# Performance work log

Measured on AMD Instinct MI355X. Metric: run time of the kernel, lower is better.

Reference implementation:

```python
import jax, jax.numpy as jnp
import numpy as np
from jax import lax

B, S, D = 2, 2048, 1024
DS, K, L = 16, 4, 6
DI = 2 * D          # expand * d_model
V, A = 32000, 7
EPS = 1e-5


def setup_inputs() -> dict:
    key = jax.random.key(0)
    ks = jax.random.split(key, 20)
    g = lambda i, shape, s=0.02: (jax.random.normal(ks[i], shape, dtype=jnp.float32) * s)
    return {
        "features": jax.random.normal(ks[0], (B, S, D), dtype=jnp.float32),
        # per-layer Mamba params, stacked on leading layer dim
        "in_proj_w": g(1, (L, D, 2 * DI)),
        "conv_w": g(2, (L, DI, K), 0.1),
        "conv_b": g(3, (L, DI), 0.0),
        "B_ssm": g(4, (L, DI, DS)),   # fixed analogs of the per-step torch.randn(d_inner,d_state)
        "C_ssm": g(5, (L, DS, DI)),   # fixed analogs of the per-step torch.randn(d_state,d_inner)
        "out_w": g(6, (L, DI, D)),
        "ln_g": jnp.ones((D,), jnp.float32),
        "ln_b": jnp.zeros((D,), jnp.float32),
        # action head (arm: 7-dof, bounds (-1,1))
        "act_w1": g(7, (D, D // 2)), "act_b1": jnp.zeros((D // 2,), jnp.float32),
        "act_w2": g(8, (D // 2, D // 4)), "act_b2": jnp.zeros((D // 4,), jnp.float32),
        "act_w3": g(9, (D // 4, A)), "act_b3": jnp.zeros((A,), jnp.float32),
        # language head
        "lang_w1": g(10, (D, D)), "lang_b1": jnp.zeros((D,), jnp.float32),
        "lang_w2": g(11, (D, V)), "lang_b2": jnp.zeros((V,), jnp.float32),
    }


def _causal_dwconv(x, w, b):
    # x: [B,S,DI], w: [DI,K], b: [DI]  -> causal depthwise conv (torch pad=K-1 then trim)
    lhs = x.transpose(0, 2, 1)                    # [B,DI,S]
    rhs = w[:, None, :]                           # [DI,1,K]
    y = lax.conv_general_dilated(lhs, rhs, window_strides=(1,),
                                 padding=[(K - 1, 0)], feature_group_count=DI,
                                 dimension_numbers=("NCH", "OIH", "NCH"))
    return (y + b[None, :, None]).transpose(0, 2, 1)  # [B,S,DI]


def _selective_scan(xc, Bm, Cm):
    # xc: [B,S,DI]; h_t = 0.9*h_{t-1} + (x_t @ Bm)*0.1 ; y_t = h_t @ Cm
    u = jnp.einsum("bsi,in->bsn", xc, Bm) * 0.1      # [B,S,DS]
    def step(h, u_t):
        h = 0.9 * h + u_t
        return h, h
    _, hs = lax.scan(step, jnp.zeros((xc.shape[0], DS), xc.dtype), u.transpose(1, 0, 2))
    return jnp.einsum("sbn,ni->bsi", hs, Cm)         # [B,S,DI]


def _mamba_block(x, in_w, cw, cb, Bm, Cm, ow):
    xz = jnp.einsum("bsd,do->bso", x, in_w)          # [B,S,2*DI]
    xp, z = xz[..., :DI], xz[..., DI:]
    xc = jax.nn.silu(_causal_dwconv(xp, cw, cb))
    y = _selective_scan(xc, Bm, Cm) * jax.nn.silu(z)
    return jnp.einsum("bsi,id->bsd", y, ow)


def _forward(features, in_proj_w, conv_w, conv_b, B_ssm, C_ssm, out_w,
             ln_g, ln_b, act_w1, act_b1, act_w2, act_b2, act_w3, act_b3,
             lang_w1, lang_b1, lang_w2, lang_b2):
    x = features
    for l in range(L):  # residual Mamba layers (fallback path: x = x + block(x))
        x = x + _mamba_block(x, in_proj_w[l], conv_w[l], conv_b[l],
                             B_ssm[l], C_ssm[l], out_w[l])
    mu = jnp.mean(x, -1, keepdims=True)
    var = jnp.mean(jnp.square(x - mu), -1, keepdims=True)
    x = (x - mu) * lax.rsqrt(var + EPS) * ln_g + ln_b
    # action head: bounds (-1,1) => affine rescale is identity
    h = jax.nn.relu(x @ act_w1 + act_b1)
    h = jax.nn.relu(h @ act_w2 + act_b2)
    actions = jnp.tanh(h @ act_w3 + act_b3)
    # language head
    logits = jax.nn.relu(x @ lang_w1 + lang_b1) @ lang_w2 + lang_b2
    return actions, logits


def reference(features, in_proj_w, conv_w, conv_b, B_ssm, C_ssm, out_w,
              ln_g, ln_b, act_w1, act_b1, act_w2, act_b2, act_w3, act_b3,
              lang_w1, lang_b1, lang_w2, lang_b2):
    return _forward(features, in_proj_w, conv_w, conv_b, B_ssm, C_ssm, out_w,
                    ln_g, ln_b, act_w1, act_b1, act_w2, act_b2, act_w3, act_b3,
                    lang_w1, lang_b1, lang_w2, lang_b2)
```

## Files before the change

### kernel.cpp

```cpp
#include <hip/hip_runtime.h>
#include <hip/hip_bf16.h>
#include <cstdint>
#include <cstddef>

#define TT 4096
#define SS 2048
#define DD 1024
#define DDI 2048
#define LL 6
#define VV 32000
#define AA 7

typedef __hip_bfloat16 bf16;
typedef __attribute__((ext_vector_type(8))) short bf16x8;
typedef __attribute__((ext_vector_type(4))) float f32x4;

typedef const __attribute__((address_space(1))) void* gas_ptr;
typedef __attribute__((address_space(3))) void* las_ptr;

static __device__ __forceinline__ float b2f(bf16 h) { return __bfloat162float(h); }
static __device__ __forceinline__ bf16 f2b(float f) { return __float2bfloat16(f); }

#define SWZ(off) ((off) ^ ((((off) >> 7) & 3) << 4))

template<int EPI>
__global__ __launch_bounds__(512, 2)
void g8_k(const bf16* __restrict__ A, const bf16* __restrict__ Wt,
          int K, int mx, int out_ld,
          float* __restrict__ of32, bf16* __restrict__ ob16,
          const float* __restrict__ bias)
{
    extern __shared__ char lds[];
    const int nwg = gridDim.x;
    int l = blockIdx.x;
    if ((nwg & 7) == 0) l = (l & 7) * (nwg >> 3) + (l >> 3);
    const int row0 = (l % mx) * 256, col0 = (l / mx) * 256;

    const int tid = threadIdx.x, wid = tid >> 6, lane = tid & 63;
    const int wr = wid >> 2, wc = wid & 3;
    const int l15 = lane & 15, kq = lane >> 4;

    f32x4 acc[8][4];
#pragma unroll
    for (int m = 0; m < 8; ++m)
#pragma unroll
        for (int n = 0; n < 4; ++n) acc[m][n] = f32x4{0.f, 0.f, 0.f, 0.f};

    const int sr   = tid >> 2;
    const int colE = (((tid & 3) ^ ((tid >> 3) & 3)) * 8);
    const bf16* gA = A  + (size_t)(row0 + sr) * K + colE;
    const bf16* gB = Wt + (size_t)(col0 + sr) * K + colE;
    const int dst0 = tid * 16, dst1 = 8192 + tid * 16;

    auto stageA = [&](int kh) {
        char* b = lds + (kh & 3) * 16384;
        __builtin_amdgcn_global_load_lds((gas_ptr)(gA + kh * 32),                   (las_ptr)(b + dst0), 16, 0, 0);
        __builtin_amdgcn_global_load_lds((gas_ptr)(gA + (size_t)128 * K + kh * 32), (las_ptr)(b + dst1), 16, 0, 0);
    };
    auto stageB = [&](int kh) {
        char* b = lds + 65536 + (kh & 3) * 16384;
        __builtin_amdgcn_global_load_lds((gas_ptr)(gB + kh * 32),                   (las_ptr)(b + dst0), 16, 0, 0);
        __builtin_amdgcn_global_load_lds((gas_ptr)(gB + (size_t)128 * K + kh * 32), (las_ptr)(b + dst1), 16, 0, 0);
    };

    const int NT = K >> 6, KH = K >> 5;
    stageA(0); stageB(0); stageA(1); stageB(1);
    stageA(2); stageB(2); stageA(3); stageB(3);
    int nextA = 4, nextB = 4;

    for (int t = 0; t < NT; ++t) {
        const char* As0 = lds + ((2 * t) & 3) * 16384;
        const char* As1 = lds + ((2 * t + 1) & 3) * 16384;
        const char* Bs0 = lds + 65536 + ((2 * t) & 3) * 16384;
        const char* Bs1 = lds + 65536 + ((2 * t + 1) & 3) * 16384;
        bf16x8 af[4], bfg[4];

        if (t < NT - 3) asm volatile("s_waitcnt vmcnt(10)" ::: "memory");
        else            asm volatile("s_waitcnt vmcnt(0)" ::: "memory");
        __builtin_amdgcn_sched_barrier(0);
        __builtin_amdgcn_s_barrier();
        __builtin_amdgcn_sched_barrier(0);
#pragma unroll
        for (int fn = 0; fn < 4; ++fn)
            bfg[fn] = *(const bf16x8*)(Bs0 + SWZ((wc * 64 + fn * 16 + l15) * 64 + kq * 16));
#pragma unroll
        for (int fm = 0; fm < 4; ++fm)
            af[fm] = *(const bf16x8*)(As0 + SWZ((wr * 128 + fm * 16 + l15) * 64 + kq * 16));
        if (t > 0 && nextA < KH) { stageA(nextA); ++nextA; }
        asm volatile("s_waitcnt lgkmcnt(0)" ::: "memory");
        __builtin_amdgcn_sched_barrier(0);
        __builtin_amdgcn_s_setprio(1);
#pragma unroll
        for (int fm = 0; fm < 4; ++fm)
#pragma unroll
            for (int fn = 0; fn < 4; ++fn)
                acc[fm][fn] = __builtin_amdgcn_mfma_f32_16x16x32_bf16(af[fm], bfg[fn], acc[fm][fn], 0, 0, 0);
        __builtin_amdgcn_s_setprio(0);
        __builtin_amdgcn_sched_barrier(0);
        __builtin_amdgcn_s_barrier();
        __builtin_amdgcn_sched_barrier(0);

#pragma unroll
        for (int fm = 0; fm < 4; ++fm)
            af[fm] = *(const bf16x8*)(As0 + SWZ((wr * 128 + 64 + fm * 16 + l15) * 64 + kq * 16));
        if (nextB < KH) { stageB(nextB); ++nextB; }
        asm volatile("s_waitcnt lgkmcnt(0)" ::: "memory");
        __builtin_amdgcn_sched_barrier(0);
        __builtin_amdgcn_s_setprio(1);
#pragma unroll
        for (int fm = 0; fm < 4; ++fm)
#pragma unroll
            for (int fn = 0; fn < 4; ++fn)
                acc[4 + fm][fn] = __builtin_amdgcn_mfma_f32_16x16x32_bf16(af[fm], bfg[fn], acc[4 + fm][fn], 0, 0, 0);
        __builtin_amdgcn_s_setprio(0);
        __builtin_amdgcn_sched_barrier(0);
        __builtin_amdgcn_s_barrier();
        __builtin_amdgcn_sched_barrier(0);

        if (t < NT - 3) asm volatile("s_waitcnt vmcnt(10)" ::: "memory");
        else            asm volatile("s_waitcnt vmcnt(0)" ::: "memory");
        __builtin_amdgcn_sched_barrier(0);
        __builtin_amdgcn_s_barrier();
        __builtin_amdgcn_sched_barrier(0);
#pragma unroll
        for (int fn = 0; fn < 4; ++fn)
            bfg[fn] = *(const bf16x8*)(Bs1 + SWZ((wc * 64 + fn * 16 + l15) * 64 + kq * 16));
#pragma unroll
        for (int fm = 0; fm < 4; ++fm)
            af[fm] = *(const bf16x8*)(As1 + SWZ((wr * 128 + fm * 16 + l15) * 64 + kq * 16));
        if (nextA < KH) { stageA(nextA); ++nextA; }
        asm volatile("s_waitcnt lgkmcnt(0)" ::: "memory");
        __builtin_amdgcn_sched_barrier(0);
        __builtin_amdgcn_s_setprio(1);
#pragma unroll
        for (int fm = 0; fm < 4; ++fm)
#pragma unroll
            for (int fn = 0; fn < 4; ++fn)
                acc[fm][fn] = __builtin_amdgcn_mfma_f32_16x16x32_bf16(af[fm], bfg[fn], acc[fm][fn], 0, 0, 0);
        __builtin_amdgcn_s_setprio(0);
        __builtin_amdgcn_sched_barrier(0);
        __builtin_amdgcn_s_barrier();
        __builtin_amdgcn_sched_barrier(0);

#pragma unroll
        for (int fm = 0; fm < 4; ++fm)
            af[fm] = *(const bf16x8*)(As1 + SWZ((wr * 128 + 64 + fm * 16 + l15) * 64 + kq * 16));
        if (nextB < KH) { stageB(nextB); ++nextB; }
        asm volatile("s_waitcnt lgkmcnt(0)" ::: "memory");
        __builtin_amdgcn_sched_barrier(0);
        __builtin_amdgcn_s_setprio(1);
#pragma unroll
        for (int fm = 0; fm < 4; ++fm)
#pragma unroll
            for (int fn = 0; fn < 4; ++fn)
                acc[4 + fm][fn] = __builtin_amdgcn_mfma_f32_16x16x32_bf16(af[fm], bfg[fn], acc[4 + fm][fn], 0, 0, 0);
        __builtin_amdgcn_s_setprio(0);
        __builtin_amdgcn_sched_barrier(0);
        __builtin_amdgcn_s_barrier();
        __builtin_amdgcn_sched_barrier(0);
    }

#pragma unroll
    for (int fm = 0; fm < 8; ++fm) {
#pragma unroll
        for (int fn = 0; fn < 4; ++fn) {
#pragma unroll
            for (int r = 0; r < 4; ++r) {
                const int row = row0 + wr * 128 + fm * 16 + kq * 4 + r;
                const int col = col0 + wc * 64 + fn * 16 + l15;
                float v = acc[fm][fn][r];
                if (EPI == 0) ob16[(size_t)row * out_ld + col] = f2b(v);
                else          of32[(size_t)row * out_ld + col] = v + bias[col];
            }
        }
    }
}

template<int EPI>
__global__ __launch_bounds__(256)
void gemm_k(const bf16* __restrict__ A, const bf16* __restrict__ Wt,
            int K, int out_ld,
            float* __restrict__ of32, bf16* __restrict__ ob16,
            const float* __restrict__ bias,
            const bf16* __restrict__ zp, int z_ld)
{
    __shared__ bf16x8 lsA8[128 * 4];
    __shared__ bf16x8 lsB8[128 * 4];
    bf16* lsA = (bf16*)lsA8;
    bf16* lsB = (bf16*)lsB8;

    const int tid  = threadIdx.x;
    const int w    = tid >> 6;
    const int lane = tid & 63;
    const int row0 = blockIdx.x * 128;
    const int col0 = blockIdx.y * 128;
    const int wr   = (w >> 1) * 64;
    const int wc   = (w & 1) * 64;
    const int l15  = lane & 15;
    const int kq   = lane >> 4;

    f32x4 acc[4][4];
#pragma unroll
    for (int m = 0; m < 4; ++m)
#pragma unroll
        for (int n = 0; n < 4; ++n) acc[m][n] = f32x4{0.f, 0.f, 0.f, 0.f};

    const int s0 = tid, s1 = tid + 256;
    const size_t ga0 = (size_t)(row0 + (s0 >> 2)) * K + (s0 & 3) * 8;
    const size_t ga1 = (size_t)(row0 + (s1 >> 2)) * K + (s1 & 3) * 8;
    const size_t gb0 = (size_t)(col0 + (s0 >> 2)) * K + (s0 & 3) * 8;
    const size_t gb1 = (size_t)(col0 + (s1 >> 2)) * K + (s1 & 3) * 8;
    bf16* la0 = lsA + (size_t)(w * 64) * 8;
    bf16* la1 = lsA + (size_t)(256 + w * 64) * 8;
    bf16* lb0 = lsB + (size_t)(w * 64) * 8;
    bf16* lb1 = lsB + (size_t)(256 + w * 64) * 8;

    for (int k0 = 0; k0 < K; k0 += 32) {
        __builtin_amdgcn_global_load_lds((gas_ptr)(A  + ga0 + k0), (las_ptr)la0, 16, 0, 0);
        __builtin_amdgcn_global_load_lds((gas_ptr)(A  + ga1 + k0), (las_ptr)la1, 16, 0, 0);
        __builtin_amdgcn_global_load_lds((gas_ptr)(Wt + gb0 + k0), (las_ptr)lb0, 16, 0, 0);
        __builtin_amdgcn_global_load_lds((gas_ptr)(Wt + gb1 + k0), (las_ptr)lb1, 16, 0, 0);
        __syncthreads();

        bf16x8 af[4], bfr[4];
#pragma unroll
        for (int m = 0; m < 4; ++m)
            af[m] = *(const bf16x8*)(lsA + (size_t)(wr + m * 16 + l15) * 32 + kq * 8);
#pragma unroll
        for (int n = 0; n < 4; ++n)
            bfr[n] = *(const bf16x8*)(lsB + (size_t)(wc + n * 16 + l15) * 32 + kq * 8);
#pragma unroll
        for (int m = 0; m < 4; ++m)
#pragma unroll
            for (int n = 0; n < 4; ++n)
                acc[m][n] = __builtin_amdgcn_mfma_f32_16x16x32_bf16(af[m], bfr[n], acc[m][n], 0, 0, 0);
        __syncthreads();
    }

#pragma unroll
    for (int m = 0; m < 4; ++m) {
#pragma unroll
        for (int n = 0; n < 4; ++n) {
#pragma unroll
            for (int r = 0; r < 4; ++r) {
                const int row = row0 + wr + m * 16 + kq * 4 + r;
                const int col = col0 + wc + n * 16 + l15;
                float v = acc[m][n][r];
                if (EPI == 2) {
                    float zf = b2f(zp[(size_t)row * z_ld + col]);
                    v *= zf / (1.f + expf(-zf));
                    ob16[(size_t)row * out_ld + col] = f2b(v);
                } else if (EPI == 3) {
                    float rr = of32[(size_t)row * out_ld + col] + v;
                    of32[(size_t)row * out_ld + col] = rr;
                    ob16[(size_t)row * out_ld + col] = f2b(rr);
                } else if (EPI == 4) {
                    v = fmaxf(v + bias[col], 0.f);
                    ob16[(size_t)row * out_ld + col] = f2b(v);
                }
            }
        }
    }
}

__global__ __launch_bounds__(256)
void usk_k(const bf16* __restrict__ A, const bf16* __restrict__ Wt,
           float* __restrict__ up)
{
    __shared__ bf16x8 lsA8[128 * 4];
    __shared__ bf16x8 lsB8[128 * 4];
    bf16* lsA = (bf16*)lsA8;
    bf16* lsB = (bf16*)lsB8;
    const int K = 2048;

    const int tid  = threadIdx.x;
    const int w    = tid >> 6;
    const int lane = tid & 63;
    const int row0 = blockIdx.x * 128;
    const int spl  = blockIdx.y;
    const int kbeg = spl * 256;
    const int wr   = (w >> 1) * 64;
    const int wc   = (w & 1) * 64;
    const int l15  = lane & 15;
    const int kq   = lane >> 4;

    f32x4 acc[4][4];
#pragma unroll
    for (int m = 0; m < 4; ++m)
#pragma unroll
        for (int n = 0; n < 4; ++n) acc[m][n] = f32x4{0.f, 0.f, 0.f, 0.f};

    const int s0 = tid, s1 = tid + 256;
    const size_t ga0 = (size_t)(row0 + (s0 >> 2)) * K + (s0 & 3) * 8;
    const size_t ga1 = (size_t)(row0 + (s1 >> 2)) * K + (s1 & 3) * 8;
    const size_t gb0 = (size_t)(s0 >> 2) * K + (s0 & 3) * 8;
    const size_t gb1 = (size_t)(s1 >> 2) * K + (s1 & 3) * 8;
    bf16* la0 = lsA + (size_t)(w * 64) * 8;
    bf16* la1 = lsA + (size_t)(256 + w * 64) * 8;
    bf16* lb0 = lsB + (size_t)(w * 64) * 8;
    bf16* lb1 = lsB + (size_t)(256 + w * 64) * 8;

    for (int k0 = kbeg; k0 < kbeg + 256; k0 += 32) {
        __builtin_amdgcn_global_load_lds((gas_ptr)(A  + ga0 + k0), (las_ptr)la0, 16, 0, 0);
        __builtin_amdgcn_global_load_lds((gas_ptr)(A  + ga1 + k0), (las_ptr)la1, 16, 0, 0);
        __builtin_amdgcn_global_load_lds((gas_ptr)(Wt + gb0 + k0), (las_ptr)lb0, 16, 0, 0);
        __builtin_amdgcn_global_load_lds((gas_ptr)(Wt + gb1 + k0), (las_ptr)lb1, 16, 0, 0);
        __syncthreads();

        bf16x8 af[4], bfr[4];
#pragma unroll
        for (int m = 0; m < 4; ++m)
            af[m] = *(const bf16x8*)(lsA + (size_t)(wr + m * 16 + l15) * 32 + kq * 8);
#pragma unroll
        for (int n = 0; n < 4; ++n)
            bfr[n] = *(const bf16x8*)(lsB + (size_t)(wc + n * 16 + l15) * 32 + kq * 8);
#pragma unroll
        for (int m = 0; m < 4; ++m)
#pragma unroll
            for (int n = 0; n < 4; ++n)
                acc[m][n] = __builtin_amdgcn_mfma_f32_16x16x32_bf16(af[m], bfr[n], acc[m][n], 0, 0, 0);
        __syncthreads();
    }

    if (wc == 0) {
#pragma unroll
        for (int m = 0; m < 4; ++m)
#pragma unroll
            for (int r = 0; r < 4; ++r) {
                const int row = row0 + wr + m * 16 + kq * 4 + r;
                up[(size_t)spl * TT * 16 + (size_t)row * 16 + l15] = acc[m][0][r];
            }
    }
}

__global__ void ured_k(const float* __restrict__ up, float* __restrict__ u)
{
    int i = blockIdx.x * 256 + threadIdx.x;
    float s = 0.f;
#pragma unroll
    for (int k = 0; k < 8; ++k) s += up[(size_t)k * TT * 16 + i];
    u[i] = s;
}

__global__ __launch_bounds__(256)
void transpose_k(const float* __restrict__ W, bf16* __restrict__ WT, int K, int N)
{
    __shared__ bf16 t[64][66];
    const int k0 = blockIdx.x * 64, n0 = blockIdx.y * 64;
    const int tid = threadIdx.x;
#pragma unroll
    for (int i = 0; i < 16; ++i) {
        int idx = i * 256 + tid;
        int kk = idx >> 6, nn = idx & 63;
        t[nn][kk] = f2b(W[(size_t)(k0 + kk) * N + n0 + nn]);
    }
    __syncthreads();
#pragma unroll
    for (int i = 0; i < 16; ++i) {
        int idx = i * 256 + tid;
        int nn = idx >> 6, kk = idx & 63;
        WT[(size_t)(n0 + nn) * K + k0 + kk] = t[nn][kk];
    }
}

__global__ void prep_bm_k(const float* __restrict__ Bm, bf16* __restrict__ BmT)
{
    int idx = blockIdx.x * 256 + threadIdx.x;
    int n = idx >> 11, k = idx & 2047;
    float v = (n < 16) ? Bm[(size_t)k * 16 + n] * 0.1f : 0.f;
    BmT[idx] = f2b(v);
}

__global__ void prep_cm_k(const float* __restrict__ Cm, bf16* __restrict__ CmT)
{
    int idx = blockIdx.x * 256 + threadIdx.x;
    int i = idx >> 5, k = idx & 31;
    float v = (k < 16) ? Cm[(size_t)k * 2048 + i] : 0.f;
    CmT[idx] = f2b(v);
}

__global__ void copyfeat_k(const float* __restrict__ f, float* __restrict__ xf,
                           bf16* __restrict__ xb)
{
    int i = (blockIdx.x * 256 + threadIdx.x) * 4;
    float4 v = *(const float4*)(f + i);
    *(float4*)(xf + i) = v;
    xb[i + 0] = f2b(v.x);
    xb[i + 1] = f2b(v.y);
    xb[i + 2] = f2b(v.z);
    xb[i + 3] = f2b(v.w);
}

__global__ void conv_k(const bf16* __restrict__ xz, const float* __restrict__ cw,
                       const float* __restrict__ cb, bf16* __restrict__ xc)
{
    int idx = blockIdx.x * 256 + threadIdx.x;
    int t = idx >> 11, i = idx & 2047;
    int s = t & (SS - 1);
    float4 wv = *(const float4*)(cw + i * 4);
    float acc = cb[i];
    const bf16* base = xz + (size_t)t * 4096 + i;
    if (s >= 3) {
        acc = fmaf(b2f(base[-3 * 4096]), wv.x, acc);
        acc = fmaf(b2f(base[-2 * 4096]), wv.y, acc);
        acc = fmaf(b2f(base[-1 * 4096]), wv.z, acc);
    } else {
        if (s >= 2) acc = fmaf(b2f(base[-2 * 4096]), wv.y, acc);
        if (s >= 1) acc = fmaf(b2f(base[-1 * 4096]), wv.z, acc);
    }
    acc = fmaf(b2f(base[0]), wv.w, acc);
    float sig = 1.f / (1.f + expf(-acc));
    xc[idx] = f2b(acc * sig);
}

__global__ void scan2_k(const float* __restrict__ u, bf16* __restrict__ hs)
{
    int gid = blockIdx.x * 256 + threadIdx.x;
    int n = gid & 15, c = (gid >> 4) & 63, b = gid >> 10;
    int start = c * 32;
    const float* ub = u + (size_t)b * SS * 16;
    bf16* hb = hs + (size_t)b * SS * 32;
    float h = 0.f;
    int w0 = start - 96; if (w0 < 0) w0 = 0;
    for (int t = w0; t < start; ++t) h = 0.9f * h + ub[(size_t)t * 16 + n];
    const bf16 zero = f2b(0.f);
    for (int t = start; t < start + 32; ++t) {
        h = 0.9f * h + ub[(size_t)t * 16 + n];
        hb[(size_t)t * 32 + n] = f2b(h);
        hb[(size_t)t * 32 + 16 + n] = zero;
    }
}

__global__ __launch_bounds__(256)
void ln_k(const float* __restrict__ x, const float* __restrict__ g,
          const float* __restrict__ bb, bf16* __restrict__ xn)
{
    int t = blockIdx.x, tid = threadIdx.x;
    const float* xr = x + (size_t)t * DD;
    float4 v = *(const float4*)(xr + tid * 4);
    float s = v.x + v.y + v.z + v.w;
#pragma unroll
    for (int o = 32; o > 0; o >>= 1) s += __shfl_down(s, o, 64);
    __shared__ float r1[4], r2[4];
    if ((tid & 63) == 0) r1[tid >> 6] = s;
    __syncthreads();
    float mu = (r1[0] + r1[1] + r1[2] + r1[3]) * (1.f / DD);
    float d0 = v.x - mu, d1 = v.y - mu, d2 = v.z - mu, d3 = v.w - mu;
    float ss = d0 * d0 + d1 * d1 + d2 * d2 + d3 * d3;
#pragma unroll
    for (int o = 32; o > 0; o >>= 1) ss += __shfl_down(ss, o, 64);
    if ((tid & 63) == 0) r2[tid >> 6] = ss;
    __syncthreads();
    float var = (r2[0] + r2[1] + r2[2] + r2[3]) * (1.f / DD);
    float inv = rsqrtf(var + 1e-5f);
    int di = tid * 4;
    xn[(size_t)t * DD + di + 0] = f2b(d0 * inv * g[di + 0] + bb[di + 0]);
    xn[(size_t)t * DD + di + 1] = f2b(d1 * inv * g[di + 1] + bb[di + 1]);
    xn[(size_t)t * DD + di + 2] = f2b(d2 * inv * g[di + 2] + bb[di + 2]);
    xn[(size_t)t * DD + di + 3] = f2b(d3 * inv * g[di + 3] + bb[di + 3]);
}

__global__ void act3_k(const bf16* __restrict__ h2, const float* __restrict__ w3,
                       const float* __restrict__ b3, float* __restrict__ out)
{
    int idx = blockIdx.x * 256 + threadIdx.x;
    if (idx >= TT * AA) return;
    int t = idx / AA, a = idx - t * AA;
    float acc = b3[a];
    const bf16* hr = h2 + (size_t)t * 256;
    for (int k = 0; k < 256; ++k)
        acc = fmaf(b2f(hr[k]), w3[k * AA + a], acc);
    out[idx] = tanhf(acc);
}

extern "C" void kernel_launch(void* const* d_in, const int* in_sizes, int n_in,
                              void* d_out, int out_size, void* d_ws, size_t ws_size,
                              hipStream_t stream)
{
    (void)in_sizes; (void)n_in; (void)out_size; (void)ws_size;
    const float* features = (const float*)d_in[0];
    const float* in_proj_w = (const float*)d_in[1];
    const float* conv_w = (const float*)d_in[2];
    const float* conv_b = (const float*)d_in[3];
    const float* B_ssm = (const float*)d_in[4];
    const float* C_ssm = (const float*)d_in[5];
    const float* out_w = (const float*)d_in[6];
    const float* ln_g = (const float*)d_in[7];
    const float* ln_b = (const float*)d_in[8];
    const float* act_w1 = (const float*)d_in[9];
    const float* act_b1 = (const float*)d_in[10];
    const float* act_w2 = (const float*)d_in[11];
    const float* act_b2 = (const float*)d_in[12];
    const float* act_w3 = (const float*)d_in[13];
    const float* act_b3 = (const float*)d_in[14];
    const float* lang_w1 = (const float*)d_in[15];
    const float* lang_b1 = (const float*)d_in[16];
    const float* lang_w2 = (const float*)d_in[17];
    const float* lang_b2 = (const float*)d_in[18];

    static bool attr_done = false;
    if (!attr_done) {
        hipFuncSetAttribute((const void*)&g8_k<0>, hipFuncAttributeMaxDynamicSharedMemorySize, 131072);
        hipFuncSetAttribute((const void*)&g8_k<5>, hipFuncAttributeMaxDynamicSharedMemorySize, 131072);
        attr_done = true;
    }

    char* p = (char*)d_ws;
    size_t off = 0;
    auto alloc = [&](size_t bytes) -> void* {
        void* q = p + off;
        off = (off + bytes + 255) & ~(size_t)255;
        return q;
    };
    float* x_f  = (float*)alloc((size_t)TT * DD * 4);
    bf16*  x_b  = (bf16*) alloc((size_t)TT * DD * 2);
    bf16*  xz   = (bf16*) alloc((size_t)TT * 4096 * 2);
    bf16*  xc   = (bf16*) alloc((size_t)TT * DDI * 2);
    float* u    = (float*)alloc((size_t)TT * 16 * 4);
    float* up   = (float*)alloc((size_t)8 * TT * 16 * 4);
    bf16*  hs   = (bf16*) alloc((size_t)TT * 32 * 2);
    bf16*  xn   = (bf16*) alloc((size_t)TT * DD * 2);
    bf16*  h1   = (bf16*) alloc((size_t)TT * 512 * 2);
    bf16*  h2   = (bf16*) alloc((size_t)TT * 256 * 2);
    bf16*  hl   = (bf16*) alloc((size_t)TT * DD * 2);
    bf16*  inwT = (bf16*) alloc((size_t)LL * 4096 * 1024 * 2);
    bf16*  owT  = (bf16*) alloc((size_t)LL * 1024 * 2048 * 2);
    bf16*  bmT  = (bf16*) alloc((size_t)LL * 128 * 2048 * 2);
    bf16*  cmT  = (bf16*) alloc((size_t)LL * 2048 * 32 * 2);
    bf16*  a1T  = (bf16*) alloc((size_t)512 * 1024 * 2);
    bf16*  a2T  = (bf16*) alloc((size_t)256 * 512 * 2);
    bf16*  l1T  = (bf16*) alloc((size_t)1024 * 1024 * 2);
    bf16*  l2T  = (bf16*) alloc((size_t)VV * 1024 * 2);
    bf16*  y    = xc;

    copyfeat_k<<<TT * DD / 1024, 256, 0, stream>>>(features, x_f, x_b);
    for (int l = 0; l < LL; ++l) {
        transpose_k<<<dim3(16, 64), 256, 0, stream>>>(in_proj_w + (size_t)l * 1024 * 4096,
                                                      inwT + (size_t)l * 4096 * 1024, 1024, 4096);
        transpose_k<<<dim3(32, 16), 256, 0, stream>>>(out_w + (size_t)l * 2048 * 1024,
                                                      owT + (size_t)l * 1024 * 2048, 2048, 1024);
        prep_bm_k<<<(128 * 2048) / 256, 256, 0, stream>>>(B_ssm + (size_t)l * 2048 * 16,
                                                          bmT + (size_t)l * 128 * 2048);
        prep_cm_k<<<(2048 * 32) / 256, 256, 0, stream>>>(C_ssm + (size_t)l * 16 * 2048,
                                                         cmT + (size_t)l * 2048 * 32);
    }
    transpose_k<<<dim3(16, 8), 256, 0, stream>>>(act_w1, a1T, 1024, 512);
    transpose_k<<<dim3(8, 4), 256, 0, stream>>>(act_w2, a2T, 512, 256);
    transpose_k<<<dim3(16, 16), 256, 0, stream>>>(lang_w1, l1T, 1024, 1024);
    transpose_k<<<dim3(16, 500), 256, 0, stream>>>(lang_w2, l2T, 1024, VV);

    for (int l = 0; l < LL; ++l) {
        g8_k<0><<<256, 512, 131072, stream>>>(x_b, inwT + (size_t)l * 4096 * 1024,
                                              1024, 16, 4096, nullptr, xz, nullptr);
        conv_k<<<TT * DDI / 256, 256, 0, stream>>>(xz, conv_w + (size_t)l * DDI * 4,
                                                   conv_b + (size_t)l * DDI, xc);
        usk_k<<<dim3(32, 8), 256, 0, stream>>>(xc, bmT + (size_t)l * 128 * 2048, up);
        ured_k<<<TT * 16 / 256, 256, 0, stream>>>(up, u);
        scan2_k<<<8, 256, 0, stream>>>(u, hs);
        gemm_k<2><<<dim3(32, 16), 256, 0, stream>>>(hs, cmT + (size_t)l * 2048 * 32,
                                                    32, 2048, nullptr, y, nullptr, xz + 2048, 4096);
        gemm_k<3><<<dim3(32, 8), 256, 0, stream>>>(y, owT + (size_t)l * 1024 * 2048,
                                                   2048, 1024, x_f, x_b, nullptr, nullptr, 0);
    }

    ln_k<<<TT, 256, 0, stream>>>(x_f, ln_g, ln_b, xn);
    gemm_k<4><<<dim3(32, 4), 256, 0, stream>>>(xn, a1T, 1024, 512, nullptr, h1, act_b1, nullptr, 0);
    gemm_k<4><<<dim3(32, 2), 256, 0, stream>>>(h1, a2T, 512, 256, nullptr, h2, act_b2, nullptr, 0);
    act3_k<<<(TT * AA + 255) / 256, 256, 0, stream>>>(h2, act_w3, act_b3, (float*)d_out);
    gemm_k<4><<<dim3(32, 8), 256, 0, stream>>>(xn, l1T, 1024, 1024, nullptr, hl, lang_b1, nullptr, 0);
    g8_k<5><<<2000, 512, 131072, stream>>>(hl, l2T, 1024, 16, VV,
                                           (float*)d_out + (size_t)TT * AA, nullptr, lang_b2);
}
```

Measured before the change: 1.646 ms.

## Pipeline out-projection GEMM with async LDS loads; compute C-projection with fp32 FMA kernel

Replaces the padded K=32 MFMA GEMM for the SSM output projection (hs @ Cm with SiLU(z) gating) with a simple per-token fp32 FMA kernel that reads C_ssm directly. This removes the per-layer Cm transpose/padding prep and the hs zero padding. The out-projection residual GEMM moves from the synchronous 128x128 gemm_k to a new g8h_k kernel. g8h_k uses global_load_lds into a 5-stage swizzled LDS ring with vmcnt-based waits and setprio around the MFMAs, to overlap loads with compute. The cost is higher LDS use per block (80 KB) and more complex wait logic.

```diff
diff --git a/kernel.cpp b/kernel.cpp
--- a/kernel.cpp
+++ b/kernel.cpp
@@ -20,6 +20,10 @@
 
 static __device__ __forceinline__ float b2f(bf16 h) { return __bfloat162float(h); }
 static __device__ __forceinline__ bf16 f2b(float f) { return __float2bfloat16(f); }
+static __device__ __forceinline__ float bs2f(short x) {
+    unsigned int u = ((unsigned int)(unsigned short)x) << 16;
+    float f; __builtin_memcpy(&f, &u, 4); return f;
+}
 
 #define SWZ(off) ((off) ^ ((((off) >> 7) & 3) << 4))
 
@@ -177,12 +181,105 @@
 }
 
 template<int EPI>
+__global__ __launch_bounds__(256, 2)
+void g8h_k(const bf16* __restrict__ A, const bf16* __restrict__ Wt,
+           int K, int mx, int out_ld,
+           float* __restrict__ of32, bf16* __restrict__ ob16,
+           const float* __restrict__ bias)
+{
+    extern __shared__ char lds[];
+    const int nwg = gridDim.x;
+    int l = blockIdx.x;
+    if ((nwg & 7) == 0) l = (l & 7) * (nwg >> 3) + (l >> 3);
+    const int row0 = (l % mx) * 128, col0 = (l / mx) * 128;
+
+    const int tid = threadIdx.x, wid = tid >> 6, lane = tid & 63;
+    const int wr = wid >> 1, wc = wid & 1;
+    const int l15 = lane & 15, kq = lane >> 4;
+
+    f32x4 acc[4][4];
+#pragma unroll
+    for (int m = 0; m < 4; ++m)
+#pragma unroll
+        for (int n = 0; n < 4; ++n) acc[m][n] = f32x4{0.f, 0.f, 0.f, 0.f};
+
+    const int sr   = tid >> 2;
+    const int colE = (((tid & 3) ^ ((tid >> 3) & 3)) * 8);
+    const bf16* gA = A  + (size_t)(row0 + sr) * K + colE;
+    const bf16* gB = Wt + (size_t)(col0 + sr) * K + colE;
+    const int dst0 = tid * 16, dst1 = 4096 + tid * 16;
+
+    auto stage = [&](int kh) {
+        char* a = lds + (kh % 5) * 8192;
+        char* b = lds + 40960 + (kh % 5) * 8192;
+        __builtin_amdgcn_global_load_lds((gas_ptr)(gA + kh * 32),                  (las_ptr)(a + dst0), 16, 0, 0);
+        __builtin_amdgcn_global_load_lds((gas_ptr)(gA + (size_t)64 * K + kh * 32), (las_ptr)(a + dst1), 16, 0, 0);
+        __builtin_amdgcn_global_load_lds((gas_ptr)(gB + kh * 32),                  (las_ptr)(b + dst0), 16, 0, 0);
+        __builtin_amdgcn_global_load_lds((gas_ptr)(gB + (size_t)64 * K + kh * 32), (las_ptr)(b + dst1), 16, 0, 0);
+    };
+
+    const int KH = K >> 5;
+    stage(0); stage(1); stage(2); stage(3);
+
+    for (int kh = 0; kh < KH; ++kh) {
+        const int rem = KH - 1 - kh;
+        if (rem >= 3)      asm volatile("s_waitcnt vmcnt(12)" ::: "memory");
+        else if (rem == 2) asm volatile("s_waitcnt vmcnt(8)" ::: "memory");
+        else if (rem == 1) asm volatile("s_waitcnt vmcnt(4)" ::: "memory");
+        else               asm volatile("s_waitcnt vmcnt(0)" ::: "memory");
+        __builtin_amdgcn_sched_barrier(0);
+        __builtin_amdgcn_s_barrier();
+        __builtin_amdgcn_sched_barrier(0);
+
+        const char* As = lds + (kh % 5) * 8192;
+        const char* Bs = lds + 40960 + (kh % 5) * 8192;
+        bf16x8 af[4], bfg[4];
+#pragma unroll
+        for (int fn = 0; fn < 4; ++fn)
+            bfg[fn] = *(const bf16x8*)(Bs + SWZ((wc * 64 + fn * 16 + l15) * 64 + kq * 16));
+#pragma unroll
+        for (int fm = 0; fm < 4; ++fm)
+            af[fm] = *(const bf16x8*)(As + SWZ((wr * 64 + fm * 16 + l15) * 64 + kq * 16));
+        if (kh + 4 < KH) stage(kh + 4);
+        asm volatile("s_waitcnt lgkmcnt(0)" ::: "memory");
+        __builtin_amdgcn_sched_barrier(0);
+        __builtin_amdgcn_s_setprio(1);
+#pragma unroll
+        for (int fm = 0; fm < 4; ++fm)
+#pragma unroll
+            for (int fn = 0; fn < 4; ++fn)
+                acc[fm][fn] = __builtin_amdgcn_mfma_f32_16x16x32_bf16(af[fm], bfg[fn], acc[fm][fn], 0, 0, 0);
+        __builtin_amdgcn_s_setprio(0);
+        __builtin_amdgcn_sched_barrier(0);
+    }
+
+#pragma unroll
+    for (int fm = 0; fm < 4; ++fm) {
+#pragma unroll
+        for (int fn = 0; fn < 4; ++fn) {
+#pragma unroll
+            for (int r = 0; r < 4; ++r) {
+                const int row = row0 + wr * 64 + fm * 16 + kq * 4 + r;
+                const int col = col0 + wc * 64 + fn * 16 + l15;
+                float v = acc[fm][fn][r];
+                if (EPI == 3) {
+                    float rr = of32[(size_t)row * out_ld + col] + v;
+                    of32[(size_t)row * out_ld + col] = rr;
+                    ob16[(size_t)row * out_ld + col] = f2b(rr);
+                } else {
+                    ob16[(size_t)row * out_ld + col] = f2b(v);
+                }
+            }
+        }
+    }
+}
+
+template<int EPI>
 __global__ __launch_bounds__(256)
 void gemm_k(const bf16* __restrict__ A, const bf16* __restrict__ Wt,
             int K, int out_ld,
             float* __restrict__ of32, bf16* __restrict__ ob16,
-            const float* __restrict__ bias,
-            const bf16* __restrict__ zp, int z_ld)
+            const float* __restrict__ bias)
 {
     __shared__ bf16x8 lsA8[128 * 4];
     __shared__ bf16x8 lsB8[128 * 4];
@@ -246,18 +343,8 @@
                 const int row = row0 + wr + m * 16 + kq * 4 + r;
                 const int col = col0 + wc + n * 16 + l15;
                 float v = acc[m][n][r];
-                if (EPI == 2) {
-                    float zf = b2f(zp[(size_t)row * z_ld + col]);
-                    v *= zf / (1.f + expf(-zf));
-                    ob16[(size_t)row * out_ld + col] = f2b(v);
-                } else if (EPI == 3) {
-                    float rr = of32[(size_t)row * out_ld + col] + v;
-                    of32[(size_t)row * out_ld + col] = rr;
-                    ob16[(size_t)row * out_ld + col] = f2b(rr);
-                } else if (EPI == 4) {
-                    v = fmaxf(v + bias[col], 0.f);
-                    ob16[(size_t)row * out_ld + col] = f2b(v);
-                }
+                v = fmaxf(v + bias[col], 0.f);
+                ob16[(size_t)row * out_ld + col] = f2b(v);
             }
         }
     }
@@ -369,14 +456,6 @@
     int n = idx >> 11, k = idx & 2047;
     float v = (n < 16) ? Bm[(size_t)k * 16 + n] * 0.1f : 0.f;
     BmT[idx] = f2b(v);
-}
-
-__global__ void prep_cm_k(const float* __restrict__ Cm, bf16* __restrict__ CmT)
-{
-    int idx = blockIdx.x * 256 + threadIdx.x;
-    int i = idx >> 5, k = idx & 31;
-    float v = (k < 16) ? Cm[(size_t)k * 2048 + i] : 0.f;
-    CmT[idx] = f2b(v);
 }
 
 __global__ void copyfeat_k(const float* __restrict__ f, float* __restrict__ xf,
@@ -413,21 +492,45 @@
     xc[idx] = f2b(acc * sig);
 }
 
-__global__ void scan2_k(const float* __restrict__ u, bf16* __restrict__ hs)
+__global__ void scan2_k(const float* __restrict__ u, float* __restrict__ hs)
 {
     int gid = blockIdx.x * 256 + threadIdx.x;
     int n = gid & 15, c = (gid >> 4) & 63, b = gid >> 10;
     int start = c * 32;
     const float* ub = u + (size_t)b * SS * 16;
-    bf16* hb = hs + (size_t)b * SS * 32;
+    float* hb = hs + (size_t)b * SS * 16;
     float h = 0.f;
     int w0 = start - 96; if (w0 < 0) w0 = 0;
     for (int t = w0; t < start; ++t) h = 0.9f * h + ub[(size_t)t * 16 + n];
-    const bf16 zero = f2b(0.f);
     for (int t = start; t < start + 32; ++t) {
         h = 0.9f * h + ub[(size_t)t * 16 + n];
-        hb[(size_t)t * 32 + n] = f2b(h);
-        hb[(size_t)t * 32 + 16 + n] = zero;
+        hb[(size_t)t * 16 + n] = h;
+    }
+}
+
+__global__ __launch_bounds__(256)
+void yk_k(const float* __restrict__ hs, const float* __restrict__ Cm,
+          const bf16* __restrict__ xz, bf16* __restrict__ y)
+{
+    const int t = blockIdx.x, i0 = threadIdx.x * 8;
+    const float* h = hs + (size_t)t * 16;
+    float o[8] = {0.f, 0.f, 0.f, 0.f, 0.f, 0.f, 0.f, 0.f};
+#pragma unroll
+    for (int n = 0; n < 16; ++n) {
+        float hn = h[n];
+        const float4* c = (const float4*)(Cm + (size_t)n * DDI + i0);
+        float4 c0 = c[0], c1 = c[1];
+        o[0] = fmaf(hn, c0.x, o[0]); o[1] = fmaf(hn, c0.y, o[1]);
+        o[2] = fmaf(hn, c0.z, o[2]); o[3] = fmaf(hn, c0.w, o[3]);
+        o[4] = fmaf(hn, c1.x, o[4]); o[5] = fmaf(hn, c1.y, o[5]);
+        o[6] = fmaf(hn, c1.z, o[6]); o[7] = fmaf(hn, c1.w, o[7]);
+    }
+    bf16x8 zv = *(const bf16x8*)(xz + (size_t)t * 4096 + 2048 + i0);
+    bf16* yo = y + (size_t)t * DDI + i0;
+#pragma unroll
+    for (int j = 0; j < 8; ++j) {
+        float zf = bs2f(zv[j]);
+        yo[j] = f2b(o[j] * (zf / (1.f + expf(-zf))));
     }
 }
 
@@ -502,6 +605,7 @@
     if (!attr_done) {
         hipFuncSetAttribute((const void*)&g8_k<0>, hipFuncAttributeMaxDynamicSharedMemorySize, 131072);
         hipFuncSetAttribute((const void*)&g8_k<5>, hipFuncAttributeMaxDynamicSharedMemorySize, 131072);
+        hipFuncSetAttribute((const void*)&g8h_k<3>, hipFuncAttributeMaxDynamicSharedMemorySize, 81920);
         attr_done = true;
     }
 
@@ -518,7 +622,7 @@
     bf16*  xc   = (bf16*) alloc((size_t)TT * DDI * 2);
     float* u    = (float*)alloc((size_t)TT * 16 * 4);
     float* up   = (float*)alloc((size_t)8 * TT * 16 * 4);
-    bf16*  hs   = (bf16*) alloc((size_t)TT * 32 * 2);
+    float* hs   = (float*)alloc((size_t)TT * 16 * 4);
     bf16*  xn   = (bf16*) alloc((size_t)TT * DD * 2);
     bf16*  h1   = (bf16*) alloc((size_t)TT * 512 * 2);
     bf16*  h2   = (bf16*) alloc((size_t)TT * 256 * 2);
@@ -526,7 +630,6 @@
     bf16*  inwT = (bf16*) alloc((size_t)LL * 4096 * 1024 * 2);
     bf16*  owT  = (bf16*) alloc((size_t)LL * 1024 * 2048 * 2);
     bf16*  bmT  = (bf16*) alloc((size_t)LL * 128 * 2048 * 2);
-    bf16*  cmT  = (bf16*) alloc((size_t)LL * 2048 * 32 * 2);
     bf16*  a1T  = (bf16*) alloc((size_t)512 * 1024 * 2);
     bf16*  a2T  = (bf16*) alloc((size_t)256 * 512 * 2);
     bf16*  l1T  = (bf16*) alloc((size_t)1024 * 1024 * 2);
@@ -541,8 +644,6 @@
                                                       owT + (size_t)l * 1024 * 2048, 2048, 1024);
         prep_bm_k<<<(128 * 2048) / 256, 256, 0, stream>>>(B_ssm + (size_t)l * 2048 * 16,
                                                           bmT + (size_t)l * 128 * 2048);
-        prep_cm_k<<<(2048 * 32) / 256, 256, 0, stream>>>(C_ssm + (size_t)l * 16 * 2048,
-                                                         cmT + (size_t)l * 2048 * 32);
     }
     transpose_k<<<dim3(16, 8), 256, 0, stream>>>(act_w1, a1T, 1024, 512);
     transpose_k<<<dim3(8, 4), 256, 0, stream>>>(act_w2, a2T, 512, 256);
@@ -557,17 +658,16 @@
         usk_k<<<dim3(32, 8), 256, 0, stream>>>(xc, bmT + (size_t)l * 128 * 2048, up);
         ured_k<<<TT * 16 / 256, 256, 0, stream>>>(up, u);
         scan2_k<<<8, 256, 0, stream>>>(u, hs);
-        gemm_k<2><<<dim3(32, 16), 256, 0, stream>>>(hs, cmT + (size_t)l * 2048 * 32,
-                                                    32, 2048, nullptr, y, nullptr, xz + 2048, 4096);
-        gemm_k<3><<<dim3(32, 8), 256, 0, stream>>>(y, owT + (size_t)l * 1024 * 2048,
-                                                   2048, 1024, x_f, x_b, nullptr, nullptr, 0);
+        yk_k<<<TT, 256, 0, stream>>>(hs, C_ssm + (size_t)l * 16 * 2048, xz, y);
+        g8h_k<3><<<256, 256, 81920, stream>>>(y, owT + (size_t)l * 1024 * 2048,
+                                              2048, 32, 1024, x_f, x_b, nullptr);
     }
 
     ln_k<<<TT, 256, 0, stream>>>(x_f, ln_g, ln_b, xn);
-    gemm_k<4><<<dim3(32, 4), 256, 0, stream>>>(xn, a1T, 1024, 512, nullptr, h1, act_b1, nullptr, 0);
-    gemm_k<4><<<dim3(32, 2), 256, 0, stream>>>(h1, a2T, 512, 256, nullptr, h2, act_b2, nullptr, 0);
+    gemm_k<4><<<dim3(32, 4), 256, 0, stream>>>(xn, a1T, 1024, 512, nullptr, h1, act_b1);
+    gemm_k<4><<<dim3(32, 2), 256, 0, stream>>>(h1, a2T, 512, 256, nullptr, h2, act_b2);
     act3_k<<<(TT * AA + 255) / 256, 256, 0, stream>>>(h2, act_w3, act_b3, (float*)d_out);
-    gemm_k<4><<<dim3(32, 8), 256, 0, stream>>>(xn, l1T, 1024, 1024, nullptr, hl, lang_b1, nullptr, 0);
+    gemm_k<4><<<dim3(32, 8), 256, 0, stream>>>(xn, l1T, 1024, 1024, nullptr, hl, lang_b1);
     g8_k<5><<<2000, 512, 131072, stream>>>(hl, l2T, 1024, 16, VV,
                                            (float*)d_out + (size_t)TT * AA, nullptr, lang_b2);
 }
```

After: 1.644 ms. No clear change (-0.2%).
